# Kernel optimization log

Hardware: AMD Instinct MI355X
Metric: run time of the kernel (lower is better)

The kernel has to match this reference:

```python
import jax, jax.numpy as jnp
from jax import lax
import numpy as np

H_FEAT = 14
W_FEAT = 14
BN_EPS = 1e-5
NORM_EPS = 1e-12

def _coord_tensor():
    # Python-2 integer division as in the original repo
    c = np.zeros((H_FEAT * W_FEAT, 2), dtype=np.float32)
    for i in range(H_FEAT * W_FEAT):
        c[i, 0] = (i // W_FEAT - H_FEAT // 2) / (H_FEAT / 2.0)
        c[i, 1] = (i % W_FEAT - W_FEAT // 2) / (W_FEAT / 2.0)
    return jnp.asarray(c.reshape(1, H_FEAT, W_FEAT, 2).transpose(0, 3, 1, 2))  # [1,2,14,14]

def _l2norm(x, axis):
    n = jnp.linalg.norm(x, axis=axis, keepdims=True)
    return x / jnp.maximum(n, NORM_EPS)

def _conv2d(x, w, b, pad):
    y = lax.conv_general_dilated(x, w, (1, 1), [(pad, pad), (pad, pad)],
                                 dimension_numbers=("NCHW", "OIHW", "NCHW"))
    return y + b[None, :, None, None]

def _bn_train(x, g, b):
    m = x.mean(axis=(0, 2, 3), keepdims=True)
    v = x.var(axis=(0, 2, 3), keepdims=True)
    return (x - m) * lax.rsqrt(v + BN_EPS) * g[None, :, None, None] + b[None, :, None, None]

def _lstm_scan(emb, Wih, Whh, bih, bhh):
    # emb: [T, B, 300]; PyTorch gate order i,f,g,o
    Hdim = Whh.shape[1]
    B = emb.shape[1]
    def step(carry, x):
        h, c = carry
        gates = x @ Wih.T + h @ Whh.T + bih + bhh  # [B, 4H]
        i, f, g, o = jnp.split(gates, 4, axis=-1)
        c = jax.nn.sigmoid(f) * c + jax.nn.sigmoid(i) * jnp.tanh(g)
        h = jax.nn.sigmoid(o) * jnp.tanh(c)
        return (h, c), h
    init = (jnp.zeros((B, Hdim), emb.dtype), jnp.zeros((B, Hdim), emb.dtype))
    _, hs = lax.scan(step, init, emb)
    return hs  # [T, B, H]

def _resblock(v, coord, c1w, c1b, c2w, c2b, bng, bnb):
    B = v.shape[0]
    vin = jnp.concatenate([v, jnp.broadcast_to(coord, (B, 2, H_FEAT, W_FEAT))], axis=1)
    v1 = jax.nn.relu(_conv2d(vin, c1w, c1b, 0))
    v2 = jax.nn.relu(_bn_train(_conv2d(v1, c2w, c2b, 1), bng, bnb))
    return v2 + v1

def setup_inputs() -> dict:
    key = jax.random.key(0)
    ks = jax.random.split(key, 24)
    B, T, V, E = 128, 45, 10000, 300
    Hh = 1024
    s = 0.02
    inp = {}
    inp["que"] = jax.random.randint(ks[0], (B, T), 0, V, dtype=jnp.int64)
    inp["img"] = jax.random.normal(ks[1], (B, 1024, H_FEAT, W_FEAT), dtype=jnp.float32)
    inp["lookup"] = s * jax.random.normal(ks[2], (V + 1, E), dtype=jnp.float32)
    inp["Wih_f"] = s * jax.random.normal(ks[3], (4 * Hh, E), dtype=jnp.float32)
    inp["Whh_f"] = s * jax.random.normal(ks[4], (4 * Hh, Hh), dtype=jnp.float32)
    inp["bih_f"] = jnp.zeros((4 * Hh,), jnp.float32)
    inp["bhh_f"] = jnp.zeros((4 * Hh,), jnp.float32)
    inp["Wih_b"] = s * jax.random.normal(ks[5], (4 * Hh, E), dtype=jnp.float32)
    inp["Whh_b"] = s * jax.random.normal(ks[6], (4 * Hh, Hh), dtype=jnp.float32)
    inp["bih_b"] = jnp.zeros((4 * Hh,), jnp.float32)
    inp["bhh_b"] = jnp.zeros((4 * Hh,), jnp.float32)
    inp["conv0_w"] = s * jax.random.normal(ks[7], (128, 1026, 3, 3), dtype=jnp.float32)
    inp["conv0_b"] = jnp.zeros((128,), jnp.float32)
    inp["bn0_g"] = jnp.ones((128,), jnp.float32)
    inp["bn0_b"] = jnp.zeros((128,), jnp.float32)
    inp["r1c1_w"] = s * jax.random.normal(ks[8], (128, 130, 1, 1), dtype=jnp.float32)
    inp["r1c1_b"] = jnp.zeros((128,), jnp.float32)
    inp["r1c2_w"] = s * jax.random.normal(ks[9], (128, 128, 3, 3), dtype=jnp.float32)
    inp["r1c2_b"] = jnp.zeros((128,), jnp.float32)
    inp["r1bn_g"] = jnp.ones((128,), jnp.float32)
    inp["r1bn_b"] = jnp.zeros((128,), jnp.float32)
    inp["r2c1_w"] = s * jax.random.normal(ks[10], (128, 130, 1, 1), dtype=jnp.float32)
    inp["r2c1_b"] = jnp.zeros((128,), jnp.float32)
    inp["r2c2_w"] = s * jax.random.normal(ks[11], (128, 128, 3, 3), dtype=jnp.float32)
    inp["r2c2_b"] = jnp.zeros((128,), jnp.float32)
    inp["r2bn_g"] = jnp.ones((128,), jnp.float32)
    inp["r2bn_b"] = jnp.zeros((128,), jnp.float32)
    return inp

def reference(que, img, lookup, Wih_f, Whh_f, bih_f, bhh_f, Wih_b, Whh_b, bih_b, bhh_b,
              conv0_w, conv0_b, bn0_g, bn0_b,
              r1c1_w, r1c1_b, r1c2_w, r1c2_b, r1bn_g, r1bn_b,
              r2c1_w, r2c1_b, r2c2_w, r2c2_b, r2bn_g, r2bn_b):
    coord = _coord_tensor()
    # ---- encoder (LSTM mode) ----
    emb = lookup[que]                      # [B, T, 300]
    emb = jnp.transpose(emb, (1, 0, 2))    # [T, B, 300]
    h_f = _lstm_scan(emb, Wih_f, Whh_f, bih_f, bhh_f)
    h_b = _lstm_scan(emb[::-1], Wih_b, Whh_b, bih_b, bhh_b)[::-1]
    qenc = _l2norm(jnp.concatenate([h_f, h_b], axis=-1), axis=-1)  # [T, B, 2048]
    enc = qenc[-1]                                                  # [B, 2048]
    # ---- image branch ----
    v = _l2norm(img, axis=1)               # per-pixel L2 norm over 1024 channels
    B = v.shape[0]
    v = jnp.concatenate([v, jnp.broadcast_to(coord, (B, 2, H_FEAT, W_FEAT))], axis=1)
    v = jax.nn.relu(_bn_train(_conv2d(v, conv0_w, conv0_b, 1), bn0_g, bn0_b))
    v = _resblock(v, coord, r1c1_w, r1c1_b, r1c2_w, r1c2_b, r1bn_g, r1bn_b)
    v = _resblock(v, coord, r2c1_w, r2c1_b, r2c2_w, r2c2_b, r2bn_g, r2bn_b)
    return (enc, v)
```

## Files before the change

### kernel.cpp

```cpp
#include <hip/hip_runtime.h>
#include <math.h>

#define BB   128
#define T    45
#define E    300
#define HH   1024
#define G4   4096
#define HW   196
#define NPX  (BB*HW)
#define C0   1026
#define CM   128
#define CR   130

static __device__ __forceinline__ float sigm(float x) { return 1.f / (1.f + __expf(-x)); }

__global__ void k_embed(const int* __restrict__ que, const float* __restrict__ lookup,
                        float* __restrict__ emb) {
    int idx = blockIdx.x * 256 + threadIdx.x;
    if (idx >= T * BB * E) return;
    int e = idx % E;
    int n = idx / E;
    int b = n % BB;
    int t = n / BB;
    int q = que[b * T + t];
    emb[idx] = lookup[(size_t)q * E + e];
}

template <int BM, int BN, int TM, int TN>
__global__ __launch_bounds__(256) void k_gemm_nt(
    const float* __restrict__ A, int lda,
    const float* __restrict__ Bw, int ldb,
    const float* __restrict__ add,
    const float* __restrict__ bias,
    float* __restrict__ C, int ldc,
    int M, int N, int K, int relu) {
    constexpr int KT = 16;
    constexpr int TX = BN / TN;
    constexpr int TY = BM / TM;
    __shared__ float As[KT][BM + 4];
    __shared__ float Bs[KT][BN + 4];
    const int tid = threadIdx.x;
    const int tx = tid % TX, ty = tid / TX;
    const int r0 = blockIdx.x * BM, c0 = blockIdx.y * BN;
    float acc[TM][TN] = {};
    for (int k0 = 0; k0 < K; k0 += KT) {
#pragma unroll
        for (int l = tid; l < BM * KT; l += 256) {
            int m = l / KT, k = l % KT;
            int gm = r0 + m, gk = k0 + k;
            As[k][m] = (gm < M && gk < K) ? A[(size_t)gm * lda + gk] : 0.f;
        }
#pragma unroll
        for (int l = tid; l < BN * KT; l += 256) {
            int n = l / KT, k = l % KT;
            int gn = c0 + n, gk = k0 + k;
            Bs[k][n] = (gn < N && gk < K) ? Bw[(size_t)gn * ldb + gk] : 0.f;
        }
        __syncthreads();
#pragma unroll
        for (int k = 0; k < KT; ++k) {
            float ar[TM], br[TN];
#pragma unroll
            for (int i = 0; i < TM; ++i) ar[i] = As[k][ty * TM + i];
#pragma unroll
            for (int j = 0; j < TN; ++j) br[j] = Bs[k][tx * TN + j];
#pragma unroll
            for (int i = 0; i < TM; ++i)
#pragma unroll
                for (int j = 0; j < TN; ++j) acc[i][j] += ar[i] * br[j];
        }
        __syncthreads();
    }
#pragma unroll
    for (int i = 0; i < TM; ++i) {
        int gm = r0 + ty * TM + i;
        if (gm >= M) continue;
#pragma unroll
        for (int j = 0; j < TN; ++j) {
            int gn = c0 + tx * TN + j;
            if (gn >= N) continue;
            float v = acc[i][j];
            if (add) v += add[(size_t)gm * ldc + gn];
            if (bias) v += bias[gn];
            if (relu) v = fmaxf(v, 0.f);
            C[(size_t)gm * ldc + gn] = v;
        }
    }
}

__global__ void k_pack_wf(const float* __restrict__ Whh, const float* __restrict__ Wih,
                          float* __restrict__ out) {
    int idx = blockIdx.x * 256 + threadIdx.x;
    if (idx >= G4 * 1328) return;
    int k = idx % 1328;
    int n = idx / 1328;
    int j = n >> 2, g = n & 3;
    int row = g * HH + j;
    float v;
    if (k < HH) v = Whh[(size_t)row * HH + k];
    else {
        int e = k - HH;
        v = (e < E) ? Wih[(size_t)row * E + e] : 0.f;
    }
    out[idx] = v;
}
__global__ void k_pack_wb(const float* __restrict__ Wih, float* __restrict__ out) {
    int idx = blockIdx.x * 256 + threadIdx.x;
    if (idx >= G4 * 304) return;
    int k = idx % 304;
    int n = idx / 304;
    int j = n >> 2, g = n & 3;
    out[idx] = (k < E) ? Wih[(size_t)(g * HH + j) * E + k] : 0.f;
}
__global__ void k_pack_b4(const float* __restrict__ bih, const float* __restrict__ bhh,
                          float* __restrict__ out) {
    int idx = blockIdx.x * 256 + threadIdx.x;
    if (idx >= G4) return;
    int j = idx >> 2, g = idx & 3;
    out[idx] = bih[g * HH + j] + bhh[g * HH + j];
}

__global__ __launch_bounds__(256) void k_lstm_fused(
    const float* __restrict__ h_in, float* __restrict__ c_io,
    const float* __restrict__ emb_t,
    const float* __restrict__ Wpk, int KP,
    const float* __restrict__ b4,
    float* __restrict__ h_out, int first) {
    __shared__ float As[16][36];
    __shared__ float Bs[16][68];
    const int tid = threadIdx.x;
    const int tx = tid & 15, ty = tid >> 4;
    const int r0 = blockIdx.x * 32;
    const int c0 = blockIdx.y * 64;
    const int xoff = KP - 304;
    const int k0s = first ? xoff : 0;
    const int ka = tid & 15, ma = tid >> 4;
    float acc[2][4] = {};
    float rA0, rA1, rB0, rB1, rB2, rB3;

#define LSTM_LD(K0)                                                               \
    {                                                                             \
        int gk = (K0) + ka;                                                       \
        if (gk < xoff) {                                                          \
            rA0 = h_in[(size_t)(r0 + ma) * HH + gk];                              \
            rA1 = h_in[(size_t)(r0 + ma + 16) * HH + gk];                         \
        } else {                                                                  \
            int e = gk - xoff;                                                    \
            rA0 = (e < E) ? emb_t[(size_t)(r0 + ma) * E + e] : 0.f;               \
            rA1 = (e < E) ? emb_t[(size_t)(r0 + ma + 16) * E + e] : 0.f;          \
        }                                                                         \
        const float* wp = Wpk + (size_t)(c0 + ma) * KP + gk;                      \
        rB0 = wp[0];                                                              \
        rB1 = wp[(size_t)16 * KP];                                                \
        rB2 = wp[(size_t)32 * KP];                                                \
        rB3 = wp[(size_t)48 * KP];                                                \
    }

    LSTM_LD(k0s);
    for (int k0 = k0s; k0 < KP; k0 += 16) {
        As[ka][ma] = rA0;
        As[ka][ma + 16] = rA1;
        Bs[ka][ma] = rB0;
        Bs[ka][ma + 16] = rB1;
        Bs[ka][ma + 32] = rB2;
        Bs[ka][ma + 48] = rB3;
        __syncthreads();
        if (k0 + 16 < KP) LSTM_LD(k0 + 16);
#pragma unroll
        for (int k = 0; k < 16; ++k) {
            float a0 = As[k][ty * 2], a1 = As[k][ty * 2 + 1];
            float br[4];
#pragma unroll
            for (int j = 0; j < 4; ++j) br[j] = Bs[k][tx * 4 + j];
#pragma unroll
            for (int j = 0; j < 4; ++j) {
                acc[0][j] += a0 * br[j];
                acc[1][j] += a1 * br[j];
            }
        }
        __syncthreads();
    }
#undef LSTM_LD
    const int jj = blockIdx.y * 16 + tx;
#pragma unroll
    for (int i = 0; i < 2; ++i) {
        int b = r0 + ty * 2 + i;
        float gi = acc[i][0] + b4[jj * 4 + 0];
        float gf = acc[i][1] + b4[jj * 4 + 1];
        float gg = acc[i][2] + b4[jj * 4 + 2];
        float go = acc[i][3] + b4[jj * 4 + 3];
        float cp = first ? 0.f : c_io[(size_t)b * HH + jj];
        float cn = sigm(gf) * cp + sigm(gi) * tanhf(gg);
        c_io[(size_t)b * HH + jj] = cn;
        h_out[(size_t)b * HH + jj] = sigm(go) * tanhf(cn);
    }
}

__global__ void k_enc(const float* __restrict__ hf, const float* __restrict__ hb,
                      float* __restrict__ out) {
    int b = blockIdx.x;
    int tid = threadIdx.x;
    float vals[8];
    float ss = 0.f;
#pragma unroll
    for (int i = 0; i < 8; ++i) {
        int j = i * 256 + tid;
        float v = (j < HH) ? hf[(size_t)b * HH + j] : hb[(size_t)b * HH + (j - HH)];
        vals[i] = v;
        ss += v * v;
    }
    __shared__ float red[256];
    red[tid] = ss;
    __syncthreads();
    for (int s = 128; s > 0; s >>= 1) {
        if (tid < s) red[tid] += red[tid + s];
        __syncthreads();
    }
    float scale = 1.f / fmaxf(sqrtf(red[0]), 1e-12f);
#pragma unroll
    for (int i = 0; i < 8; ++i) out[(size_t)b * 2048 + i * 256 + tid] = vals[i] * scale;
}

__global__ void k_pixssq(const float* __restrict__ img, float* __restrict__ ssq) {
    int b = blockIdx.x >> 4;
    int cc = (blockIdx.x & 15) * 64;
    int p = threadIdx.x;
    if (p >= HW) return;
    const float* base = img + ((size_t)b * 1024 + cc) * HW + p;
    float acc = 0.f;
#pragma unroll 4
    for (int c = 0; c < 64; ++c) {
        float v = base[(size_t)c * HW];
        acc += v * v;
    }
    atomicAdd(&ssq[b * HW + p], acc);
}

__global__ void k_invn(float* __restrict__ ssq) {
    int i = blockIdx.x * 256 + threadIdx.x;
    if (i >= NPX) return;
    ssq[i] = 1.f / fmaxf(sqrtf(ssq[i]), 1e-12f);
}

__global__ void k_packB0(const float* __restrict__ w, float* __restrict__ o) {
    int idx = blockIdx.x * 256 + threadIdx.x;
    if (idx >= 8 * 9 * 1040 * 16) return;
    int oi = idx & 15;
    int r = idx >> 4;
    int c = r % 1040;
    int gt = r / 1040;
    int tap = gt % 9, ocg = gt / 9;
    o[idx] = (c < C0) ? w[((size_t)(ocg * 16 + oi) * C0 + c) * 9 + tap] : 0.f;
}
__global__ void k_packBpm(const float* __restrict__ w, float* __restrict__ o) {
    int idx = blockIdx.x * 256 + threadIdx.x;
    if (idx >= 8 * 9 * 128 * 16) return;
    int oi = idx & 15;
    int r = idx >> 4;
    int c = r % 128;
    int gt = r / 128;
    int tap = gt % 9, ocg = gt / 9;
    o[idx] = w[((size_t)(ocg * 16 + oi) * 128 + c) * 9 + tap];
}

__global__ __launch_bounds__(256) void k_conv0(const float* __restrict__ img,
                                               const float* __restrict__ invn,
                                               const float* __restrict__ wpk,
                                               const float* __restrict__ bias,
                                               float* __restrict__ out) {
    __shared__ float As[289][20];
    const int tid = threadIdx.x;
    const int P0 = blockIdx.x * 256;
    const int g = P0 + tid;
    const int ocg = blockIdx.y;
    const int p = g % HW;
    const int y = p / 14, x = p % 14;
    float acc[16] = {};
    if (tid < 16) As[288][tid] = 0.f;
    for (int k0 = 0; k0 < 1040; k0 += 16) {
        __syncthreads();
        for (int l = tid; l < 288 * 16; l += 256) {
            int s = l % 288, k = l / 288;
            int gp = P0 - 16 + s;
            float v = 0.f;
            if (gp >= 0 && gp < NPX) {
                int gk = k0 + k;
                int pp = gp % HW;
                if (gk < 1024) v = img[((size_t)(gp / HW) * 1024 + gk) * HW + pp] * invn[gp];
                else if (gk == 1024) v = (float)(pp / 14 - 7) * (1.f / 7.f);
                else if (gk == 1025) v = (float)(pp % 14 - 7) * (1.f / 7.f);
            }
            As[s][k] = v;
        }
        __syncthreads();
        for (int tap = 0; tap < 9; ++tap) {
            const int ky = tap / 3 - 1, kx = tap % 3 - 1;
            const int yy = y + ky, xx = x + kx;
            const int of = ((unsigned)yy < 14u && (unsigned)xx < 14u)
                               ? (tid + 16 + ky * 14 + kx) : 288;
            const float4* __restrict__ wq =
                (const float4*)wpk + ((size_t)(ocg * 9 + tap) * 1040 + k0) * 4;
            for (int kq = 0; kq < 4; ++kq) {
                float4 a4 = *(const float4*)&As[of][kq * 4];
                float av[4] = {a4.x, a4.y, a4.z, a4.w};
#pragma unroll
                for (int kk = 0; kk < 4; ++kk) {
                    float a = av[kk];
                    float4 w0 = wq[0], w1 = wq[1], w2 = wq[2], w3 = wq[3];
                    wq += 4;
                    acc[0]  += a * w0.x;  acc[1]  += a * w0.y;
                    acc[2]  += a * w0.z;  acc[3]  += a * w0.w;
                    acc[4]  += a * w1.x;  acc[5]  += a * w1.y;
                    acc[6]  += a * w1.z;  acc[7]  += a * w1.w;
                    acc[8]  += a * w2.x;  acc[9]  += a * w2.y;
                    acc[10] += a * w2.z;  acc[11] += a * w2.w;
                    acc[12] += a * w3.x;  acc[13] += a * w3.y;
                    acc[14] += a * w3.z;  acc[15] += a * w3.w;
                }
            }
        }
    }
    float* op = out + (size_t)g * CM + ocg * 16;
    const float* bp = bias + ocg * 16;
#pragma unroll
    for (int q = 0; q < 4; ++q) {
        float4 r;
        r.x = acc[q * 4 + 0] + bp[q * 4 + 0];
        r.y = acc[q * 4 + 1] + bp[q * 4 + 1];
        r.z = acc[q * 4 + 2] + bp[q * 4 + 2];
        r.w = acc[q * 4 + 3] + bp[q * 4 + 3];
        *(float4*)&op[q * 4] = r;
    }
}

__global__ __launch_bounds__(256) void k_conv_pm(const float* __restrict__ vin,
                                                 const float* __restrict__ wpk,
                                                 const float* __restrict__ bias,
                                                 float* __restrict__ out) {
    __shared__ float As[289][20];
    const int tid = threadIdx.x;
    const int P0 = blockIdx.x * 256;
    const int g = P0 + tid;
    const int ocg = blockIdx.y;
    const int p = g % HW;
    const int y = p / 14, x = p % 14;
    float acc[16] = {};
    if (tid < 16) As[288][tid] = 0.f;
    for (int k0 = 0; k0 < CM; k0 += 16) {
        __syncthreads();
        for (int l = tid; l < 288 * 4; l += 256) {
            int s = l >> 2, kq = l & 3;
            int gp = P0 - 16 + s;
            float4 v;
            v.x = v.y = v.z = v.w = 0.f;
            if (gp >= 0 && gp < NPX) v = *(const float4*)&vin[(size_t)gp * CM + k0 + kq * 4];
            *(float4*)&As[s][kq * 4] = v;
        }
        __syncthreads();
        for (int tap = 0; tap < 9; ++tap) {
            const int ky = tap / 3 - 1, kx = tap % 3 - 1;
            const int yy = y + ky, xx = x + kx;
            const int of = ((unsigned)yy < 14u && (unsigned)xx < 14u)
                               ? (tid + 16 + ky * 14 + kx) : 288;
            const float4* __restrict__ wq =
                (const float4*)wpk + ((size_t)(ocg * 9 + tap) * 128 + k0) * 4;
            for (int kq = 0; kq < 4; ++kq) {
                float4 a4 = *(const float4*)&As[of][kq * 4];
                float av[4] = {a4.x, a4.y, a4.z, a4.w};
#pragma unroll
                for (int kk = 0; kk < 4; ++kk) {
                    float a = av[kk];
                    float4 w0 = wq[0], w1 = wq[1], w2 = wq[2], w3 = wq[3];
                    wq += 4;
                    acc[0]  += a * w0.x;  acc[1]  += a * w0.y;
                    acc[2]  += a * w0.z;  acc[3]  += a * w0.w;
                    acc[4]  += a * w1.x;  acc[5]  += a * w1.y;
                    acc[6]  += a * w1.z;  acc[7]  += a * w1.w;
                    acc[8]  += a * w2.x;  acc[9]  += a * w2.y;
                    acc[10] += a * w2.z;  acc[11] += a * w2.w;
                    acc[12] += a * w3.x;  acc[13] += a * w3.y;
                    acc[14] += a * w3.z;  acc[15] += a * w3.w;
                }
            }
        }
    }
    float* op = out + (size_t)g * CM + ocg * 16;
    const float* bp = bias + ocg * 16;
#pragma unroll
    for (int q = 0; q < 4; ++q) {
        float4 r;
        r.x = acc[q * 4 + 0] + bp[q * 4 + 0];
        r.y = acc[q * 4 + 1] + bp[q * 4 + 1];
        r.z = acc[q * 4 + 2] + bp[q * 4 + 2];
        r.w = acc[q * 4 + 3] + bp[q * 4 + 3];
        *(float4*)&op[q * 4] = r;
    }
}

__global__ void k_bnstats(const float* __restrict__ x, float* __restrict__ stats) {
    int r0 = blockIdx.x * 224;
    int c = threadIdx.x & 127, rh = threadIdx.x >> 7;
    float s = 0.f, ss = 0.f;
    for (int r = r0 + rh; r < r0 + 224; r += 2) {
        float v = x[(size_t)r * CM + c];
        s += v;
        ss += v * v;
    }
    __shared__ float rs[256], rss[256];
    rs[threadIdx.x] = s;
    rss[threadIdx.x] = ss;
    __syncthreads();
    if (threadIdx.x < 128) {
        s = rs[threadIdx.x] + rs[threadIdx.x + 128];
        ss = rss[threadIdx.x] + rss[threadIdx.x + 128];
        atomicAdd(&stats[c], s);
        atomicAdd(&stats[128 + c], ss);
    }
}

__global__ void k_bnfinal(const float* __restrict__ stats, const float* __restrict__ g,
                          const float* __restrict__ b, float* __restrict__ scsh) {
    int c = threadIdx.x;
    if (c >= 128) return;
    float mean = stats[c] / (float)NPX;
    float var = stats[128 + c] / (float)NPX - mean * mean;
    float sc = g[c] * rsqrtf(var + 1e-5f);
    scsh[c] = sc;
    scsh[128 + c] = b[c] - mean * sc;
}

__global__ void k_apply_cat(const float* __restrict__ x, const float* __restrict__ scsh,
                            const float* __restrict__ addv, float* __restrict__ vinr) {
    int idx = blockIdx.x * 256 + threadIdx.x;
    if (idx >= NPX * CM) return;
    int c = idx & 127;
    int p = idx >> 7;
    float v = fmaxf(x[idx] * scsh[c] + scsh[128 + c], 0.f);
    if (addv) v += addv[idx];
    vinr[(size_t)p * CR + c] = v;
}

__global__ void k_coords_r(float* __restrict__ vinr) {
    int p = blockIdx.x * 256 + threadIdx.x;
    if (p >= NPX) return;
    int pp = p % HW;
    int y = pp / 14, x = pp % 14;
    vinr[(size_t)p * CR + 128] = (float)(y - 7) * (1.f / 7.f);
    vinr[(size_t)p * CR + 129] = (float)(x - 7) * (1.f / 7.f);
}

__global__ void k_final(const float* __restrict__ x, const float* __restrict__ scsh,
                        const float* __restrict__ addv, float* __restrict__ outv) {
    int idx = blockIdx.x * 256 + threadIdx.x;
    if (idx >= NPX * CM) return;
    int p = idx % HW;
    int o = (idx / HW) & 127;
    int b = idx / (HW * CM);
    size_t pm = ((size_t)b * HW + p) * CM + o;
    outv[idx] = fmaxf(x[pm] * scsh[o] + scsh[128 + o], 0.f) + addv[pm];
}

extern "C" void kernel_launch(void* const* d_in, const int* in_sizes, int n_in,
                              void* d_out, int out_size, void* d_ws, size_t ws_size,
                              hipStream_t stream) {
    const int* que = (const int*)d_in[0];
    const float* img = (const float*)d_in[1];
    const float* lookup = (const float*)d_in[2];
    const float* Wih_f = (const float*)d_in[3];
    const float* Whh_f = (const float*)d_in[4];
    const float* bih_f = (const float*)d_in[5];
    const float* bhh_f = (const float*)d_in[6];
    const float* Wih_b = (const float*)d_in[7];
    const float* Whh_b = (const float*)d_in[8];
    const float* bih_b = (const float*)d_in[9];
    const float* bhh_b = (const float*)d_in[10];
    const float* conv0_w = (const float*)d_in[11];
    const float* conv0_b = (const float*)d_in[12];
    const float* bn0_g = (const float*)d_in[13];
    const float* bn0_b = (const float*)d_in[14];
    const float* r1c1_w = (const float*)d_in[15];
    const float* r1c1_b = (const float*)d_in[16];
    const float* r1c2_w = (const float*)d_in[17];
    const float* r1c2_b = (const float*)d_in[18];
    const float* r1bn_g = (const float*)d_in[19];
    const float* r1bn_b = (const float*)d_in[20];
    const float* r2c1_w = (const float*)d_in[21];
    const float* r2c1_b = (const float*)d_in[22];
    const float* r2c2_w = (const float*)d_in[23];
    const float* r2c2_b = (const float*)d_in[24];
    const float* r2bn_g = (const float*)d_in[25];
    const float* r2bn_b = (const float*)d_in[26];
    float* out = (float*)d_out;

    float* ws = (float*)d_ws;
    float* emb = ws;
    float* WfPk = emb + 1728000;
    float* WbPk = WfPk + 5439488;
    float* b4f = WbPk + 1245184;
    float* b4b = b4f + 4096;
    float* hA = b4b + 4096;
    float* hB = hA + 131072;
    float* cbuf = hB + 131072;
    float* hbb = cbuf + 131072;
    size_t lstm_end = (size_t)(hbb + 131072 - ws);
    float* invn = ws;
    float* wpk0 = invn + 25088;
    float* wpk1 = wpk0 + 1198080;
    float* wpk2 = wpk1 + 147456;
    float* x0 = wpk2 + 147456;
    float* vinr = x0 + 3211264;
    float* v1 = vinr + 3261440;
    float* v2pre = v1 + 3211264;
    float* stats = v2pre + 3211264;
    float* scsh = stats + 256;
    size_t img_end = (size_t)(scsh + 256 - ws);
    size_t need = (lstm_end > img_end ? lstm_end : img_end) * 4;
    if (ws_size < need) return;

    auto cdiv = [](int a, int b) { return (a + b - 1) / b; };

    k_embed<<<cdiv(T * BB * E, 256), 256, 0, stream>>>(que, lookup, emb);
    k_pack_wf<<<cdiv(G4 * 1328, 256), 256, 0, stream>>>(Whh_f, Wih_f, WfPk);
    k_pack_wb<<<cdiv(G4 * 304, 256), 256, 0, stream>>>(Wih_b, WbPk);
    k_pack_b4<<<cdiv(G4, 256), 256, 0, stream>>>(bih_f, bhh_f, b4f);
    k_pack_b4<<<cdiv(G4, 256), 256, 0, stream>>>(bih_b, bhh_b, b4b);
    k_lstm_fused<<<dim3(4, 64), 256, 0, stream>>>(hA, cbuf, emb + (size_t)(T - 1) * BB * E,
                                                  WbPk, 304, b4b, hbb, 1);
    float* hp = hA;
    float* hq = hB;
    float* hlast = hA;
    for (int t = 0; t < T; ++t) {
        k_lstm_fused<<<dim3(4, 64), 256, 0, stream>>>(hq, cbuf, emb + (size_t)t * BB * E,
                                                      WfPk, 1328, b4f, hp, t == 0);
        hlast = hp;
        float* tmp = hp; hp = hq; hq = tmp;
    }
    k_enc<<<128, 256, 0, stream>>>(hlast, hbb, out);

    hipMemsetAsync(invn, 0, NPX * 4, stream);
    k_pixssq<<<BB * 16, 256, 0, stream>>>(img, invn);
    k_invn<<<cdiv(NPX, 256), 256, 0, stream>>>(invn);
    k_packB0<<<cdiv(8 * 9 * 1040 * 16, 256), 256, 0, stream>>>(conv0_w, wpk0);
    k_packBpm<<<cdiv(8 * 9 * 128 * 16, 256), 256, 0, stream>>>(r1c2_w, wpk1);
    k_packBpm<<<cdiv(8 * 9 * 128 * 16, 256), 256, 0, stream>>>(r2c2_w, wpk2);

    k_conv0<<<dim3(98, 8), 256, 0, stream>>>(img, invn, wpk0, conv0_b, x0);
    hipMemsetAsync(stats, 0, 256 * 4, stream);
    k_bnstats<<<112, 256, 0, stream>>>(x0, stats);
    k_bnfinal<<<1, 128, 0, stream>>>(stats, bn0_g, bn0_b, scsh);
    k_apply_cat<<<cdiv(NPX * CM, 256), 256, 0, stream>>>(x0, scsh, nullptr, vinr);
    k_coords_r<<<cdiv(NPX, 256), 256, 0, stream>>>(vinr);

    k_gemm_nt<64, 64, 4, 4><<<dim3(392, 2), 256, 0, stream>>>(
        vinr, CR, r1c1_w, CR, nullptr, r1c1_b, v1, CM, NPX, CM, CR, 1);
    k_conv_pm<<<dim3(98, 8), 256, 0, stream>>>(v1, wpk1, r1c2_b, v2pre);
    hipMemsetAsync(stats, 0, 256 * 4, stream);
    k_bnstats<<<112, 256, 0, stream>>>(v2pre, stats);
    k_bnfinal<<<1, 128, 0, stream>>>(stats, r1bn_g, r1bn_b, scsh);
    k_apply_cat<<<cdiv(NPX * CM, 256), 256, 0, stream>>>(v2pre, scsh, v1, vinr);

    k_gemm_nt<64, 64, 4, 4><<<dim3(392, 2), 256, 0, stream>>>(
        vinr, CR, r2c1_w, CR, nullptr, r2c1_b, v1, CM, NPX, CM, CR, 1);
    k_conv_pm<<<dim3(98, 8), 256, 0, stream>>>(v1, wpk2, r2c2_b, v2pre);
    hipMemsetAsync(stats, 0, 256 * 4, stream);
    k_bnstats<<<112, 256, 0, stream>>>(v2pre, stats);
    k_bnfinal<<<1, 128, 0, stream>>>(stats, r2bn_g, r2bn_b, scsh);
    k_final<<<cdiv(NPX * CM, 256), 256, 0, stream>>>(v2pre, scsh, v1, out + (size_t)BB * 2048);
}
```

Baseline: 4.041 ms.

## Hoist LSTM input projection, split-K recurrent GEMM, and split-K convs with atomics

New measurement: 4.607 ms. +14.0%, slower.

```diff
diff --git a/kernel.cpp b/kernel.cpp
--- a/kernel.cpp
+++ b/kernel.cpp
@@ -11,6 +11,7 @@
 #define C0   1026
 #define CM   128
 #define CR   130
+#define TCH  15
 
 static __device__ __forceinline__ float sigm(float x) { return 1.f / (1.f + __expf(-x)); }
 
@@ -33,28 +34,31 @@
     const float* __restrict__ add,
     const float* __restrict__ bias,
     float* __restrict__ C, int ldc,
-    int M, int N, int K, int relu) {
+    int M, int N, int K, int relu,
+    int ksplit, size_t cstride) {
     constexpr int KT = 16;
     constexpr int TX = BN / TN;
-    constexpr int TY = BM / TM;
     __shared__ float As[KT][BM + 4];
     __shared__ float Bs[KT][BN + 4];
     const int tid = threadIdx.x;
     const int tx = tid % TX, ty = tid / TX;
     const int r0 = blockIdx.x * BM, c0 = blockIdx.y * BN;
+    const int koff = blockIdx.z * ksplit;
+    const int kend = (koff + ksplit < K) ? koff + ksplit : K;
+    C += (size_t)blockIdx.z * cstride;
     float acc[TM][TN] = {};
-    for (int k0 = 0; k0 < K; k0 += KT) {
+    for (int k0 = koff; k0 < kend; k0 += KT) {
 #pragma unroll
         for (int l = tid; l < BM * KT; l += 256) {
             int m = l / KT, k = l % KT;
             int gm = r0 + m, gk = k0 + k;
-            As[k][m] = (gm < M && gk < K) ? A[(size_t)gm * lda + gk] : 0.f;
+            As[k][m] = (gm < M && gk < kend) ? A[(size_t)gm * lda + gk] : 0.f;
         }
 #pragma unroll
         for (int l = tid; l < BN * KT; l += 256) {
             int n = l / KT, k = l % KT;
             int gn = c0 + n, gk = k0 + k;
-            Bs[k][n] = (gn < N && gk < K) ? Bw[(size_t)gn * ldb + gk] : 0.f;
+            Bs[k][n] = (gn < N && gk < kend) ? Bw[(size_t)gn * ldb + gk] : 0.f;
         }
         __syncthreads();
 #pragma unroll
@@ -88,112 +92,31 @@
     }
 }
 
-__global__ void k_pack_wf(const float* __restrict__ Whh, const float* __restrict__ Wih,
+__global__ void k_biasadd(const float* __restrict__ bih, const float* __restrict__ bhh,
                           float* __restrict__ out) {
     int idx = blockIdx.x * 256 + threadIdx.x;
-    if (idx >= G4 * 1328) return;
-    int k = idx % 1328;
-    int n = idx / 1328;
-    int j = n >> 2, g = n & 3;
-    int row = g * HH + j;
-    float v;
-    if (k < HH) v = Whh[(size_t)row * HH + k];
-    else {
-        int e = k - HH;
-        v = (e < E) ? Wih[(size_t)row * E + e] : 0.f;
-    }
-    out[idx] = v;
-}
-__global__ void k_pack_wb(const float* __restrict__ Wih, float* __restrict__ out) {
-    int idx = blockIdx.x * 256 + threadIdx.x;
-    if (idx >= G4 * 304) return;
-    int k = idx % 304;
-    int n = idx / 304;
-    int j = n >> 2, g = n & 3;
-    out[idx] = (k < E) ? Wih[(size_t)(g * HH + j) * E + k] : 0.f;
-}
-__global__ void k_pack_b4(const float* __restrict__ bih, const float* __restrict__ bhh,
-                          float* __restrict__ out) {
-    int idx = blockIdx.x * 256 + threadIdx.x;
-    if (idx >= G4) return;
-    int j = idx >> 2, g = idx & 3;
-    out[idx] = bih[g * HH + j] + bhh[g * HH + j];
-}
-
-__global__ __launch_bounds__(256) void k_lstm_fused(
-    const float* __restrict__ h_in, float* __restrict__ c_io,
-    const float* __restrict__ emb_t,
-    const float* __restrict__ Wpk, int KP,
-    const float* __restrict__ b4,
-    float* __restrict__ h_out, int first) {
-    __shared__ float As[16][36];
-    __shared__ float Bs[16][68];
-    const int tid = threadIdx.x;
-    const int tx = tid & 15, ty = tid >> 4;
-    const int r0 = blockIdx.x * 32;
-    const int c0 = blockIdx.y * 64;
-    const int xoff = KP - 304;
-    const int k0s = first ? xoff : 0;
-    const int ka = tid & 15, ma = tid >> 4;
-    float acc[2][4] = {};
-    float rA0, rA1, rB0, rB1, rB2, rB3;
-
-#define LSTM_LD(K0)                                                               \
-    {                                                                             \
-        int gk = (K0) + ka;                                                       \
-        if (gk < xoff) {                                                          \
-            rA0 = h_in[(size_t)(r0 + ma) * HH + gk];                              \
-            rA1 = h_in[(size_t)(r0 + ma + 16) * HH + gk];                         \
-        } else {                                                                  \
-            int e = gk - xoff;                                                    \
-            rA0 = (e < E) ? emb_t[(size_t)(r0 + ma) * E + e] : 0.f;               \
-            rA1 = (e < E) ? emb_t[(size_t)(r0 + ma + 16) * E + e] : 0.f;          \
-        }                                                                         \
-        const float* wp = Wpk + (size_t)(c0 + ma) * KP + gk;                      \
-        rB0 = wp[0];                                                              \
-        rB1 = wp[(size_t)16 * KP];                                                \
-        rB2 = wp[(size_t)32 * KP];                                                \
-        rB3 = wp[(size_t)48 * KP];                                                \
-    }
-
-    LSTM_LD(k0s);
-    for (int k0 = k0s; k0 < KP; k0 += 16) {
-        As[ka][ma] = rA0;
-        As[ka][ma + 16] = rA1;
-        Bs[ka][ma] = rB0;
-        Bs[ka][ma + 16] = rB1;
-        Bs[ka][ma + 32] = rB2;
-        Bs[ka][ma + 48] = rB3;
-        __syncthreads();
-        if (k0 + 16 < KP) LSTM_LD(k0 + 16);
-#pragma unroll
-        for (int k = 0; k < 16; ++k) {
-            float a0 = As[k][ty * 2], a1 = As[k][ty * 2 + 1];
-            float br[4];
-#pragma unroll
-            for (int j = 0; j < 4; ++j) br[j] = Bs[k][tx * 4 + j];
-#pragma unroll
-            for (int j = 0; j < 4; ++j) {
-                acc[0][j] += a0 * br[j];
-                acc[1][j] += a1 * br[j];
-            }
-        }
-        __syncthreads();
-    }
-#undef LSTM_LD
-    const int jj = blockIdx.y * 16 + tx;
-#pragma unroll
-    for (int i = 0; i < 2; ++i) {
-        int b = r0 + ty * 2 + i;
-        float gi = acc[i][0] + b4[jj * 4 + 0];
-        float gf = acc[i][1] + b4[jj * 4 + 1];
-        float gg = acc[i][2] + b4[jj * 4 + 2];
-        float go = acc[i][3] + b4[jj * 4 + 3];
-        float cp = first ? 0.f : c_io[(size_t)b * HH + jj];
-        float cn = sigm(gf) * cp + sigm(gi) * tanhf(gg);
-        c_io[(size_t)b * HH + jj] = cn;
-        h_out[(size_t)b * HH + jj] = sigm(go) * tanhf(cn);
-    }
+    if (idx < G4) out[idx] = bih[idx] + bhh[idx];
+}
+
+__global__ void k_cell4(float* __restrict__ h, float* __restrict__ c,
+                        const float* __restrict__ gx,
+                        const float* __restrict__ p, size_t pstride,
+                        int np, int first) {
+    int idx = blockIdx.x * 256 + threadIdx.x;
+    int b = idx >> 10, j = idx & 1023;
+    size_t base = (size_t)b * G4 + j;
+    float gi = gx[base], gf = gx[base + HH], gg = gx[base + 2 * HH], go = gx[base + 3 * HH];
+    for (int q = 0; q < np; ++q) {
+        const float* pp = p + (size_t)q * pstride;
+        gi += pp[base];
+        gf += pp[base + HH];
+        gg += pp[base + 2 * HH];
+        go += pp[base + 3 * HH];
+    }
+    float cp = first ? 0.f : c[idx];
+    float cn = sigm(gf) * cp + sigm(gi) * tanhf(gg);
+    c[idx] = cn;
+    h[idx] = sigm(go) * tanhf(cn);
 }
 
 __global__ void k_enc(const float* __restrict__ hf, const float* __restrict__ hb,
@@ -273,11 +196,12 @@
     const int P0 = blockIdx.x * 256;
     const int g = P0 + tid;
     const int ocg = blockIdx.y;
+    const int koff = blockIdx.z * 208;
     const int p = g % HW;
     const int y = p / 14, x = p % 14;
     float acc[16] = {};
     if (tid < 16) As[288][tid] = 0.f;
-    for (int k0 = 0; k0 < 1040; k0 += 16) {
+    for (int k0 = koff; k0 < koff + 208; k0 += 16) {
         __syncthreads();
         for (int l = tid; l < 288 * 16; l += 256) {
             int s = l % 288, k = l / 288;
@@ -322,15 +246,9 @@
     }
     float* op = out + (size_t)g * CM + ocg * 16;
     const float* bp = bias + ocg * 16;
-#pragma unroll
-    for (int q = 0; q < 4; ++q) {
-        float4 r;
-        r.x = acc[q * 4 + 0] + bp[q * 4 + 0];
-        r.y = acc[q * 4 + 1] + bp[q * 4 + 1];
-        r.z = acc[q * 4 + 2] + bp[q * 4 + 2];
-        r.w = acc[q * 4 + 3] + bp[q * 4 + 3];
-        *(float4*)&op[q * 4] = r;
-    }
+    const bool z0 = (blockIdx.z == 0);
+#pragma unroll
+    for (int i = 0; i < 16; ++i) atomicAdd(&op[i], acc[i] + (z0 ? bp[i] : 0.f));
 }
 
 __global__ __launch_bounds__(256) void k_conv_pm(const float* __restrict__ vin,
@@ -342,11 +260,12 @@
     const int P0 = blockIdx.x * 256;
     const int g = P0 + tid;
     const int ocg = blockIdx.y;
+    const int koff = blockIdx.z * 64;
     const int p = g % HW;
     const int y = p / 14, x = p % 14;
     float acc[16] = {};
     if (tid < 16) As[288][tid] = 0.f;
-    for (int k0 = 0; k0 < CM; k0 += 16) {
+    for (int k0 = koff; k0 < koff + 64; k0 += 16) {
         __syncthreads();
         for (int l = tid; l < 288 * 4; l += 256) {
             int s = l >> 2, kq = l & 3;
@@ -386,15 +305,9 @@
     }
     float* op = out + (size_t)g * CM + ocg * 16;
     const float* bp = bias + ocg * 16;
-#pragma unroll
-    for (int q = 0; q < 4; ++q) {
-        float4 r;
-        r.x = acc[q * 4 + 0] + bp[q * 4 + 0];
-        r.y = acc[q * 4 + 1] + bp[q * 4 + 1];
-        r.z = acc[q * 4 + 2] + bp[q * 4 + 2];
-        r.w = acc[q * 4 + 3] + bp[q * 4 + 3];
-        *(float4*)&op[q * 4] = r;
-    }
+    const bool z0 = (blockIdx.z == 0);
+#pragma unroll
+    for (int i = 0; i < 16; ++i) atomicAdd(&op[i], acc[i] + (z0 ? bp[i] : 0.f));
 }
 
 __global__ void k_bnstats(const float* __restrict__ x, float* __restrict__ stats) {
@@ -494,13 +407,13 @@
 
     float* ws = (float*)d_ws;
     float* emb = ws;
-    float* WfPk = emb + 1728000;
-    float* WbPk = WfPk + 5439488;
-    float* b4f = WbPk + 1245184;
-    float* b4b = b4f + 4096;
-    float* hA = b4b + 4096;
-    float* hB = hA + 131072;
-    float* cbuf = hB + 131072;
+    float* Xc = emb + 1728000;
+    float* Xb = Xc + 7864320;
+    float* part = Xb + 524288;
+    float* b4fp = part + 2097152;
+    float* b4bp = b4fp + 4096;
+    float* h = b4bp + 4096;
+    float* cbuf = h + 131072;
     float* hbb = cbuf + 131072;
     size_t lstm_end = (size_t)(hbb + 131072 - ws);
     float* invn = ws;
@@ -518,24 +431,30 @@
     if (ws_size < need) return;
 
     auto cdiv = [](int a, int b) { return (a + b - 1) / b; };
+    const size_t BG = (size_t)BB * G4;
 
     k_embed<<<cdiv(T * BB * E, 256), 256, 0, stream>>>(que, lookup, emb);
-    k_pack_wf<<<cdiv(G4 * 1328, 256), 256, 0, stream>>>(Whh_f, Wih_f, WfPk);
-    k_pack_wb<<<cdiv(G4 * 304, 256), 256, 0, stream>>>(Wih_b, WbPk);
-    k_pack_b4<<<cdiv(G4, 256), 256, 0, stream>>>(bih_f, bhh_f, b4f);
-    k_pack_b4<<<cdiv(G4, 256), 256, 0, stream>>>(bih_b, bhh_b, b4b);
-    k_lstm_fused<<<dim3(4, 64), 256, 0, stream>>>(hA, cbuf, emb + (size_t)(T - 1) * BB * E,
-                                                  WbPk, 304, b4b, hbb, 1);
-    float* hp = hA;
-    float* hq = hB;
-    float* hlast = hA;
+    k_biasadd<<<16, 256, 0, stream>>>(bih_f, bhh_f, b4fp);
+    k_biasadd<<<16, 256, 0, stream>>>(bih_b, bhh_b, b4bp);
+    k_gemm_nt<64, 64, 4, 4><<<dim3(2, 64, 1), 256, 0, stream>>>(
+        emb + (size_t)(T - 1) * BB * E, E, Wih_b, E, nullptr, b4bp, Xb, G4,
+        BB, G4, E, 0, E, 0);
+    k_cell4<<<512, 256, 0, stream>>>(hbb, cbuf, Xb, nullptr, 0, 0, 1);
     for (int t = 0; t < T; ++t) {
-        k_lstm_fused<<<dim3(4, 64), 256, 0, stream>>>(hq, cbuf, emb + (size_t)t * BB * E,
-                                                      WfPk, 1328, b4f, hp, t == 0);
-        hlast = hp;
-        float* tmp = hp; hp = hq; hq = tmp;
-    }
-    k_enc<<<128, 256, 0, stream>>>(hlast, hbb, out);
+        if (t % TCH == 0) {
+            k_gemm_nt<64, 64, 4, 4><<<dim3(2 * TCH, 64, 1), 256, 0, stream>>>(
+                emb + (size_t)t * BB * E, E, Wih_f, E, nullptr, b4fp, Xc, G4,
+                TCH * BB, G4, E, 0, E, 0);
+        }
+        if (t > 0) {
+            k_gemm_nt<32, 64, 2, 4><<<dim3(4, 64, 4), 256, 0, stream>>>(
+                h, HH, Whh_f, HH, nullptr, nullptr, part, G4,
+                BB, G4, HH, 0, 256, BG);
+        }
+        k_cell4<<<512, 256, 0, stream>>>(h, cbuf, Xc + (size_t)(t % TCH) * BG,
+                                         part, BG, (t > 0) ? 4 : 0, t == 0);
+    }
+    k_enc<<<128, 256, 0, stream>>>(h, hbb, out);
 
     hipMemsetAsync(invn, 0, NPX * 4, stream);
     k_pixssq<<<BB * 16, 256, 0, stream>>>(img, invn);
@@ -544,24 +463,27 @@
     k_packBpm<<<cdiv(8 * 9 * 128 * 16, 256), 256, 0, stream>>>(r1c2_w, wpk1);
     k_packBpm<<<cdiv(8 * 9 * 128 * 16, 256), 256, 0, stream>>>(r2c2_w, wpk2);
 
-    k_conv0<<<dim3(98, 8), 256, 0, stream>>>(img, invn, wpk0, conv0_b, x0);
+    hipMemsetAsync(x0, 0, (size_t)NPX * CM * 4, stream);
+    k_conv0<<<dim3(98, 8, 5), 256, 0, stream>>>(img, invn, wpk0, conv0_b, x0);
     hipMemsetAsync(stats, 0, 256 * 4, stream);
     k_bnstats<<<112, 256, 0, stream>>>(x0, stats);
     k_bnfinal<<<1, 128, 0, stream>>>(stats, bn0_g, bn0_b, scsh);
     k_apply_cat<<<cdiv(NPX * CM, 256), 256, 0, stream>>>(x0, scsh, nullptr, vinr);
     k_coords_r<<<cdiv(NPX, 256), 256, 0, stream>>>(vinr);
 
-    k_gemm_nt<64, 64, 4, 4><<<dim3(392, 2), 256, 0, stream>>>(
-        vinr, CR, r1c1_w, CR, nullptr, r1c1_b, v1, CM, NPX, CM, CR, 1);
-    k_conv_pm<<<dim3(98, 8), 256, 0, stream>>>(v1, wpk1, r1c2_b, v2pre);
+    k_gemm_nt<64, 64, 4, 4><<<dim3(392, 2, 1), 256, 0, stream>>>(
+        vinr, CR, r1c1_w, CR, nullptr, r1c1_b, v1, CM, NPX, CM, CR, 1, CR, 0);
+    hipMemsetAsync(v2pre, 0, (size_t)NPX * CM * 4, stream);
+    k_conv_pm<<<dim3(98, 8, 2), 256, 0, stream>>>(v1, wpk1, r1c2_b, v2pre);
     hipMemsetAsync(stats, 0, 256 * 4, stream);
     k_bnstats<<<112, 256, 0, stream>>>(v2pre, stats);
     k_bnfinal<<<1, 128, 0, stream>>>(stats, r1bn_g, r1bn_b, scsh);
     k_apply_cat<<<cdiv(NPX * CM, 256), 256, 0, stream>>>(v2pre, scsh, v1, vinr);
 
-    k_gemm_nt<64, 64, 4, 4><<<dim3(392, 2), 256, 0, stream>>>(
-        vinr, CR, r2c1_w, CR, nullptr, r2c1_b, v1, CM, NPX, CM, CR, 1);
-    k_conv_pm<<<dim3(98, 8), 256, 0, stream>>>(v1, wpk2, r2c2_b, v2pre);
+    k_gemm_nt<64, 64, 4, 4><<<dim3(392, 2, 1), 256, 0, stream>>>(
+        vinr, CR, r2c1_w, CR, nullptr, r2c1_b, v1, CM, NPX, CM, CR, 1, CR, 0);
+    hipMemsetAsync(v2pre, 0, (size_t)NPX * CM * 4, stream);
+    k_conv_pm<<<dim3(98, 8, 2), 256, 0, stream>>>(v1, wpk2, r2c2_b, v2pre);
     hipMemsetAsync(stats, 0, 256 * 4, stream);
     k_bnstats<<<112, 256, 0, stream>>>(v2pre, stats);
     k_bnfinal<<<1, 128, 0, stream>>>(stats, r2bn_g, r2bn_b, scsh);
```
